# Kernel optimization log

Measured on AMD Instinct MI355X. Metric: run time of the kernel, lower is better.

Reference implementation:

```python
import jax, jax.numpy as jnp
import numpy as np

B, N, IN_DIM, OUT_DIM = 4, 2048, 1024, 512


def setup_inputs() -> dict:
    key = jax.random.key(0)
    k1, k2, k3, k4, k5 = jax.random.split(key, 5)
    x = jax.random.normal(k1, (B, N, IN_DIM), dtype=jnp.float32)
    fc_w = jax.random.normal(k2, (OUT_DIM, IN_DIM), dtype=jnp.float32) * (1.0 / np.sqrt(IN_DIM))
    fc_b = jax.random.normal(k3, (OUT_DIM,), dtype=jnp.float32) * 0.01
    attn_w = jax.random.normal(k4, (1, 2 * OUT_DIM), dtype=jnp.float32) * (1.0 / np.sqrt(2 * OUT_DIM))
    attn_b = jax.random.normal(k5, (1,), dtype=jnp.float32) * 0.01
    return {"x": x, "fc_w": fc_w, "fc_b": fc_b, "attn_w": attn_w, "attn_b": attn_b}


def reference(x, fc_w, fc_b, attn_w, attn_b):
    # h = fc(x): [B, N, D]
    h = jnp.einsum('bni,di->bnd', x, fc_w) + fc_b
    D = h.shape[-1]
    # attn(cat([h_i, h_j])) == h_i @ a1 + h_j @ a2 + b  (exact factorization of
    # the Linear over the concat axis; avoids the O(N^2 * 2D) concat tensor)
    a1 = attn_w[0, :D]   # weights multiplying h_i
    a2 = attn_w[0, D:]   # weights multiplying h_j
    s1 = h @ a1          # [B, N]
    s2 = h @ a2          # [B, N]
    e = s1[:, :, None] + s2[:, None, :] + attn_b[0]  # [B, N, N]
    alpha = jax.nn.softmax(e, axis=-1)
    out = jnp.einsum('bij,bjd->bid', alpha, h)       # [B, N, D]
    return out
```

## Files before the change

kernel.cpp:

```cpp
#include <hip/hip_runtime.h>

#define BATCH 4
#define NROWS 2048
#define IN_DIM 1024
#define OUT_DIM 512
#define DSPLIT 16
#define NCHUNK 256
#define RPB 32

__global__ void __launch_bounds__(256)
k1_w2part(const float* __restrict__ fc_w,
          const float* __restrict__ attn_w,
          float* __restrict__ w2part) {
    int ds = blockIdx.x >> 2, cg = blockIdx.x & 3;
    int col = (cg << 8) + threadIdx.x;
    int d0 = ds << 5;
    float acc = 0.f;
#pragma unroll 8
    for (int j = 0; j < 32; ++j)
        acc += fc_w[(size_t)(d0 + j) * IN_DIM + col] * attn_w[OUT_DIM + d0 + j];
    w2part[(ds << 10) + col] = acc;
}

__global__ void __launch_bounds__(512)
k2_chunk(const float* __restrict__ x,
         const float* __restrict__ w2part,
         float* __restrict__ yu,
         float* __restrict__ Zc) {
    const int bid = blockIdx.x, t = threadIdx.x;
    const int w = t >> 6, lane = t & 63;
    __shared__ float w2s[IN_DIM];
    __shared__ float4 sbuf[8 * 256];
    __shared__ float zbuf[8];

    if (t < 256) {
        const float4* wp = (const float4*)w2part;
        float4 s = {0.f, 0.f, 0.f, 0.f};
#pragma unroll
        for (int ds = 0; ds < DSPLIT; ++ds) {
            float4 v = wp[(ds << 8) + t];
            s.x += v.x; s.y += v.y; s.z += v.z; s.w += v.w;
        }
        ((float4*)w2s)[t] = s;
    }
    __syncthreads();

    const float4* x4 = (const float4*)x;
    const float4* w2s4 = (const float4*)w2s;
    const float4 u0 = w2s4[lane],       u1 = w2s4[lane + 64],
                 u2 = w2s4[lane + 128], u3 = w2s4[lane + 192];

    size_t row0 = (size_t)bid * RPB + (w << 2);
    float4 a0 = {0,0,0,0}, a1 = {0,0,0,0}, a2 = {0,0,0,0}, a3 = {0,0,0,0};
    float zw = 0.f;
#pragma unroll
    for (int r = 0; r < 4; ++r) {
        size_t base = (row0 + r) << 8;
        float4 v0 = x4[base + lane];
        float4 v1 = x4[base + lane + 64];
        float4 v2 = x4[base + lane + 128];
        float4 v3 = x4[base + lane + 192];
        float d = v0.x*u0.x + v0.y*u0.y + v0.z*u0.z + v0.w*u0.w
                + v1.x*u1.x + v1.y*u1.y + v1.z*u1.z + v1.w*u1.w
                + v2.x*u2.x + v2.y*u2.y + v2.z*u2.z + v2.w*u2.w
                + v3.x*u3.x + v3.y*u3.y + v3.z*u3.z + v3.w*u3.w;
#pragma unroll
        for (int off = 32; off; off >>= 1) d += __shfl_xor(d, off, 64);
        float e = __expf(d);
        zw += e;
        a0.x += e*v0.x; a0.y += e*v0.y; a0.z += e*v0.z; a0.w += e*v0.w;
        a1.x += e*v1.x; a1.y += e*v1.y; a1.z += e*v1.z; a1.w += e*v1.w;
        a2.x += e*v2.x; a2.y += e*v2.y; a2.z += e*v2.z; a2.w += e*v2.w;
        a3.x += e*v3.x; a3.y += e*v3.y; a3.z += e*v3.z; a3.w += e*v3.w;
    }
    sbuf[(w << 8) + lane]       = a0;
    sbuf[(w << 8) + lane + 64]  = a1;
    sbuf[(w << 8) + lane + 128] = a2;
    sbuf[(w << 8) + lane + 192] = a3;
    if (lane == 0) zbuf[w] = zw;
    __syncthreads();

    if (t < 256) {
        float4 s = {0.f, 0.f, 0.f, 0.f};
#pragma unroll
        for (int i = 0; i < 8; ++i) {
            float4 v = sbuf[(i << 8) + t];
            s.x += v.x; s.y += v.y; s.z += v.z; s.w += v.w;
        }
        ((float4*)(yu + ((size_t)bid << 10)))[t] = s;
        if (t == 0) {
            float z = 0.f;
#pragma unroll
            for (int i = 0; i < 8; ++i) z += zbuf[i];
            Zc[bid] = z;
        }
    }
}

__global__ void __launch_bounds__(256)
k3_fused(const float* __restrict__ yu,
         const float* __restrict__ Zc,
         const float* __restrict__ fc_w,
         const float* __restrict__ fc_b,
         float4* __restrict__ out) {
    const int bid = blockIdx.x;
    const int b = bid >> 6, rem = bid & 63, ds = rem >> 2, rg = rem & 3;
    const int t = threadIdx.x, w = t >> 6, lane = t & 63;
    __shared__ float ys[IN_DIM];
    __shared__ float cs[32];
    __shared__ float zsh;

    if (w == 0) {
        float z = Zc[(b << 6) + lane];
#pragma unroll
        for (int off = 32; off; off >>= 1) z += __shfl_xor(z, off, 64);
        if (lane == 0) zsh = 1.f / z;
    }

    const float4* yu4 = (const float4*)yu + ((size_t)b << 14);
    float4 acc = {0.f, 0.f, 0.f, 0.f};
#pragma unroll 8
    for (int c = 0; c < 64; ++c) {
        float4 v = yu4[(c << 8) + t];
        acc.x += v.x; acc.y += v.y; acc.z += v.z; acc.w += v.w;
    }
    __syncthreads();
    const float invZ = zsh;
    acc.x *= invZ; acc.y *= invZ; acc.z *= invZ; acc.w *= invZ;
    ((float4*)ys)[t] = acc;
    __syncthreads();

    const float4* ys4 = (const float4*)ys;
    const float4 y0 = ys4[lane],       y1 = ys4[lane + 64],
                 y2 = ys4[lane + 128], y3 = ys4[lane + 192];
#pragma unroll
    for (int q = 0; q < 8; ++q) {
        int dl = (w << 3) + q;
        int d = (ds << 5) + dl;
        const float4* fr = (const float4*)fc_w + ((size_t)d << 8);
        float4 f0 = fr[lane], f1 = fr[lane + 64], f2 = fr[lane + 128], f3 = fr[lane + 192];
        float s = f0.x*y0.x + f0.y*y0.y + f0.z*y0.z + f0.w*y0.w
                + f1.x*y1.x + f1.y*y1.y + f1.z*y1.z + f1.w*y1.w
                + f2.x*y2.x + f2.y*y2.y + f2.z*y2.z + f2.w*y2.w
                + f3.x*y3.x + f3.y*y3.y + f3.z*y3.z + f3.w*y3.w;
#pragma unroll
        for (int off = 32; off; off >>= 1) s += __shfl_xor(s, off, 64);
        if (lane == 0) cs[dl] = s + fc_b[d];
    }
    __syncthreads();

    const float4 val = ((const float4*)cs)[t & 7];
    const int lr = t >> 3;
    size_t rowbase = ((size_t)b * NROWS + (rg << 9) + lr) * 128 + (ds << 3) + (t & 7);
#pragma unroll
    for (int it = 0; it < 16; ++it)
        out[rowbase + (size_t)it * 32 * 128] = val;
}

extern "C" void kernel_launch(void* const* d_in, const int* in_sizes, int n_in,
                              void* d_out, int out_size, void* d_ws, size_t ws_size,
                              hipStream_t stream) {
    const float* x      = (const float*)d_in[0];
    const float* fc_w   = (const float*)d_in[1];
    const float* fc_b   = (const float*)d_in[2];
    const float* attn_w = (const float*)d_in[3];

    float* wsf    = (float*)d_ws;
    float* w2part = wsf;
    float* Zc     = w2part + DSPLIT * IN_DIM;
    float* yu     = Zc + NCHUNK;
    float* out    = (float*)d_out;

    k1_w2part<<<64,     256, 0, stream>>>(fc_w, attn_w, w2part);
    k2_chunk <<<NCHUNK, 512, 0, stream>>>(x, w2part, yu, Zc);
    k3_fused <<<256,    256, 0, stream>>>(yu, Zc, fc_w, fc_b, (float4*)out);
}
```

Measured before the change: 31.47 us.

## Fuse w2 partial reduction into chunk kernel with atomic-counter grid sync

The separate w2part kernel is removed. Its work now runs in the first 32 blocks of the chunk kernel, each of which signals a global counter with a release atomic. All blocks issue their x loads into registers first, then spin on an acquire load until every producer has finished, so the x fetch overlaps the w2 computation and one kernel launch boundary goes away. A hipMemsetAsync is added to reset the counter on each call. The spin-wait relies on all producer blocks being resident at the same time, and holding x in registers raises register pressure.

```diff
diff --git a/kernel.cpp b/kernel.cpp
--- a/kernel.cpp
+++ b/kernel.cpp
@@ -5,73 +5,90 @@
 #define IN_DIM 1024
 #define OUT_DIM 512
 #define DSPLIT 16
+#define NPROD 32
 #define NCHUNK 256
 #define RPB 32
 
-__global__ void __launch_bounds__(256)
-k1_w2part(const float* __restrict__ fc_w,
-          const float* __restrict__ attn_w,
-          float* __restrict__ w2part) {
-    int ds = blockIdx.x >> 2, cg = blockIdx.x & 3;
-    int col = (cg << 8) + threadIdx.x;
-    int d0 = ds << 5;
-    float acc = 0.f;
-#pragma unroll 8
-    for (int j = 0; j < 32; ++j)
-        acc += fc_w[(size_t)(d0 + j) * IN_DIM + col] * attn_w[OUT_DIM + d0 + j];
-    w2part[(ds << 10) + col] = acc;
-}
+#define LD_ACQ(p)    __hip_atomic_load((p), __ATOMIC_ACQUIRE, __HIP_MEMORY_SCOPE_AGENT)
+#define ADD_REL(p,v) __hip_atomic_fetch_add((p), (v), __ATOMIC_RELEASE, __HIP_MEMORY_SCOPE_AGENT)
 
 __global__ void __launch_bounds__(512)
-k2_chunk(const float* __restrict__ x,
-         const float* __restrict__ w2part,
+d1_fused(const float* __restrict__ x,
+         const float* __restrict__ fc_w,
+         const float* __restrict__ attn_w,
+         unsigned int* __restrict__ w2cnt,
+         float* __restrict__ w2part,
          float* __restrict__ yu,
-         float* __restrict__ Zc) {
+         float* __restrict__ Zc)
+{
     const int bid = blockIdx.x, t = threadIdx.x;
     const int w = t >> 6, lane = t & 63;
     __shared__ float w2s[IN_DIM];
     __shared__ float4 sbuf[8 * 256];
     __shared__ float zbuf[8];
 
+    if (bid < NPROD) {
+        const int ds = bid >> 1;
+        const int col = ((bid & 1) << 9) + t;
+        const int d0 = ds << 5;
+        float acc = 0.f;
+#pragma unroll 8
+        for (int j = 0; j < 32; ++j)
+            acc += fc_w[(size_t)(d0 + j) * IN_DIM + col] * attn_w[OUT_DIM + d0 + j];
+        w2part[(ds << 10) + col] = acc;
+        __syncthreads();
+        if (t == 0) ADD_REL(w2cnt, 1u);
+    }
+
+    const float4* x4 = (const float4*)x;
+    const size_t row0 = (size_t)bid * RPB + (w << 2);
+    float4 v0[4], v1[4], v2[4], v3[4];
+#pragma unroll
+    for (int r = 0; r < 4; ++r) {
+        size_t base = (row0 + r) << 8;
+        v0[r] = x4[base + lane];
+        v1[r] = x4[base + lane + 64];
+        v2[r] = x4[base + lane + 128];
+        v3[r] = x4[base + lane + 192];
+    }
+#pragma unroll
+    for (int r = 0; r < 4; ++r)
+        asm volatile("" :: "v"(v0[r].x), "v"(v1[r].x), "v"(v2[r].x), "v"(v3[r].x));
+
+    if (t == 0) { while (LD_ACQ(w2cnt) < NPROD) __builtin_amdgcn_s_sleep(8); }
+    __syncthreads();
+
     if (t < 256) {
         const float4* wp = (const float4*)w2part;
         float4 s = {0.f, 0.f, 0.f, 0.f};
 #pragma unroll
         for (int ds = 0; ds < DSPLIT; ++ds) {
-            float4 v = wp[(ds << 8) + t];
-            s.x += v.x; s.y += v.y; s.z += v.z; s.w += v.w;
+            float4 q = wp[(ds << 8) + t];
+            s.x += q.x; s.y += q.y; s.z += q.z; s.w += q.w;
         }
         ((float4*)w2s)[t] = s;
     }
     __syncthreads();
 
-    const float4* x4 = (const float4*)x;
     const float4* w2s4 = (const float4*)w2s;
     const float4 u0 = w2s4[lane],       u1 = w2s4[lane + 64],
                  u2 = w2s4[lane + 128], u3 = w2s4[lane + 192];
-
-    size_t row0 = (size_t)bid * RPB + (w << 2);
     float4 a0 = {0,0,0,0}, a1 = {0,0,0,0}, a2 = {0,0,0,0}, a3 = {0,0,0,0};
     float zw = 0.f;
 #pragma unroll
     for (int r = 0; r < 4; ++r) {
-        size_t base = (row0 + r) << 8;
-        float4 v0 = x4[base + lane];
-        float4 v1 = x4[base + lane + 64];
-        float4 v2 = x4[base + lane + 128];
-        float4 v3 = x4[base + lane + 192];
-        float d = v0.x*u0.x + v0.y*u0.y + v0.z*u0.z + v0.w*u0.w
-                + v1.x*u1.x + v1.y*u1.y + v1.z*u1.z + v1.w*u1.w
-                + v2.x*u2.x + v2.y*u2.y + v2.z*u2.z + v2.w*u2.w
-                + v3.x*u3.x + v3.y*u3.y + v3.z*u3.z + v3.w*u3.w;
+        float d = v0[r].x*u0.x + v0[r].y*u0.y + v0[r].z*u0.z + v0[r].w*u0.w
+                + v1[r].x*u1.x + v1[r].y*u1.y + v1[r].z*u1.z + v1[r].w*u1.w
+                + v2[r].x*u2.x + v2[r].y*u2.y + v2[r].z*u2.z + v2[r].w*u2.w
+                + v3[r].x*u3.x + v3[r].y*u3.y + v3[r].z*u3.z + v3[r].w*u3.w;
 #pragma unroll
         for (int off = 32; off; off >>= 1) d += __shfl_xor(d, off, 64);
         float e = __expf(d);
         zw += e;
-        a0.x += e*v0.x; a0.y += e*v0.y; a0.z += e*v0.z; a0.w += e*v0.w;
-        a1.x += e*v1.x; a1.y += e*v1.y; a1.z += e*v1.z; a1.w += e*v1.w;
-        a2.x += e*v2.x; a2.y += e*v2.y; a2.z += e*v2.z; a2.w += e*v2.w;
-        a3.x += e*v3.x; a3.y += e*v3.y; a3.z += e*v3.z; a3.w += e*v3.w;
+        a0.x += e*v0[r].x; a0.y += e*v0[r].y; a0.z += e*v0[r].z; a0.w += e*v0[r].w;
+        a1.x += e*v1[r].x; a1.y += e*v1[r].y; a1.z += e*v1[r].z; a1.w += e*v1[r].w;
+        a2.x += e*v2[r].x; a2.y += e*v2[r].y; a2.z += e*v2[r].z; a2.w += e*v2[r].w;
+        a3.x += e*v3[r].x; a3.y += e*v3[r].y; a3.z += e*v3[r].z; a3.w += e*v3[r].w;
     }
     sbuf[(w << 8) + lane]       = a0;
     sbuf[(w << 8) + lane + 64]  = a1;
@@ -84,8 +101,8 @@
         float4 s = {0.f, 0.f, 0.f, 0.f};
 #pragma unroll
         for (int i = 0; i < 8; ++i) {
-            float4 v = sbuf[(i << 8) + t];
-            s.x += v.x; s.y += v.y; s.z += v.z; s.w += v.w;
+            float4 q = sbuf[(i << 8) + t];
+            s.x += q.x; s.y += q.y; s.z += q.z; s.w += q.w;
         }
         ((float4*)(yu + ((size_t)bid << 10)))[t] = s;
         if (t == 0) {
@@ -165,13 +182,14 @@
     const float* fc_b   = (const float*)d_in[2];
     const float* attn_w = (const float*)d_in[3];
 
-    float* wsf    = (float*)d_ws;
-    float* w2part = wsf;
+    unsigned int* flags = (unsigned int*)d_ws;
+    float* fbase  = (float*)(flags + 16);
+    float* w2part = fbase;
     float* Zc     = w2part + DSPLIT * IN_DIM;
     float* yu     = Zc + NCHUNK;
     float* out    = (float*)d_out;
 
-    k1_w2part<<<64,     256, 0, stream>>>(fc_w, attn_w, w2part);
-    k2_chunk <<<NCHUNK, 512, 0, stream>>>(x, w2part, yu, Zc);
-    k3_fused <<<256,    256, 0, stream>>>(yu, Zc, fc_w, fc_b, (float4*)out);
+    hipMemsetAsync(flags, 0, 64, stream);
+    d1_fused<<<NCHUNK, 512, 0, stream>>>(x, fc_w, attn_w, flags, w2part, yu, Zc);
+    k3_fused<<<256,    256, 0, stream>>>(yu, Zc, fc_w, fc_b, (float4*)out);
 }
```

New measurement: 41.31 us. 1.31x slower.
